# Kernel optimization log

Measured on AMD Instinct MI355X. Metric: run time of the kernel, lower is better.

The kernel has to match this reference:

```python
import jax, jax.numpy as jnp
import numpy as np

H = 300  # hidden size hardcoded in the module
VX = 32000
VY = 32000
NX, NY, B = 128, 128, 256


def setup_inputs() -> dict:
    key = jax.random.key(0)
    ks = jax.random.split(key, 10)
    s = 1.0 / np.sqrt(H)
    x = jax.random.randint(ks[0], (NX, B), 0, VX)
    y = jax.random.randint(ks[1], (NY, B), 0, VY)
    # padding_idx=0: zero the pad row of each embedding table
    enc_emb = jax.random.normal(ks[2], (VX, H), jnp.float32).at[0].set(0.0)
    encW = jax.random.uniform(ks[3], (H, H), jnp.float32, -s, s)
    encb = jax.random.uniform(ks[4], (H,), jnp.float32, -s, s)
    dec_emb = jax.random.normal(ks[5], (VY, H), jnp.float32).at[0].set(0.0)
    decW = jax.random.uniform(ks[6], (H, H), jnp.float32, -s, s)
    decb = jax.random.uniform(ks[7], (H,), jnp.float32, -s, s)
    outW = jax.random.uniform(ks[8], (VY, H), jnp.float32, -s, s)
    outb = jax.random.uniform(ks[9], (VY,), jnp.float32, -s, s)
    return {"x": x, "y": y, "enc_emb": enc_emb, "encW": encW, "encb": encb,
            "dec_emb": dec_emb, "decW": decW, "decb": decb,
            "outW": outW, "outb": outb}


def reference(x, y, enc_emb, encW, encb, dec_emb, decW, decb, outW, outb):
    # Encoder: Elman recurrence h = relu(e_x[i] + W h + b)
    e_x = enc_emb[x]                                  # [NX, B, H]
    h0 = jnp.zeros((x.shape[1], H), e_x.dtype)        # h=0 broadcast over batch

    def enc_step(h, ex):
        return jax.nn.relu(ex + h @ encW.T + encb), None

    h, _ = jax.lax.scan(enc_step, h0, e_x)

    # Decoder: teacher-forced recurrence with per-step mean cross-entropy
    e_y = dec_emb[y]                                  # [NY, B, H]

    def dec_step(h, inp):
        ey, tgt = inp
        h = jax.nn.relu(ey + h @ decW.T + decb)
        logits = h @ outW.T + outb                    # [B, VY]
        logp = jax.nn.log_softmax(logits, axis=-1)
        ce = -jnp.mean(jnp.take_along_axis(logp, tgt[:, None], axis=-1))
        return h, ce

    _, ces = jax.lax.scan(dec_step, h, (e_y[:-1], y[1:]))
    return jnp.sum(ces)
```

## Files before the change

kernel.cpp:

```cpp
#include <hip/hip_runtime.h>
#include <hip/hip_bf16.h>
#include <stdint.h>

typedef unsigned short u16;
typedef unsigned char u8;
typedef float f32x4 __attribute__((ext_vector_type(4)));
typedef float f32x2 __attribute__((ext_vector_type(2)));
typedef _Float16 f16x2 __attribute__((ext_vector_type(2)));
typedef _Float16 f16x8 __attribute__((ext_vector_type(8)));

#define H      300
#define KP     320
#define BATCH  256
#define NX     128
#define NY     128
#define VY     32000
#define NPAD   32768
#define MROWS  32512


#define OWS_OFF   0UL
#define OWS_BYTES ((unsigned long)NPAD * KP)
#define OWS_PAD   131072UL
#define A8_OFF    (OWS_OFF + OWS_BYTES + OWS_PAD)
#define A8_BYTES  ((unsigned long)MROWS * KP)
#define WTE_OFF   (A8_OFF + A8_BYTES)
#define WT_BYTES  (320UL * KP * 4)
#define WTD_OFF   (WTE_OFF + WT_BYTES)
#define OBP_OFF   (WTD_OFF + WT_BYTES)
#define OBP_BYTES ((unsigned long)NPAD * 4)
#define SE_OFF    (OBP_OFF + OBP_BYTES)
#define SE_BYTES  ((unsigned long)MROWS * 4)
#define EE_OFF    (SE_OFF + SE_BYTES)
#define E1_BYTES  ((unsigned long)NX * BATCH * 320 * 2)
#define ED_OFF    (EE_OFF + E1_BYTES)
#define WS_NEED   (ED_OFF + E1_BYTES)

#define ASYNC_COPY16(dst_lds, src_glb)                                          \
    __builtin_amdgcn_global_load_lds(                                           \
        (const __attribute__((address_space(1))) unsigned int*)(src_glb),       \
        (__attribute__((address_space(3))) unsigned int*)(dst_lds), 16, 0, 0)

__global__ __launch_bounds__(256) void k0_prep(const float* __restrict__ outW,
                                               const float* __restrict__ encW,
                                               const float* __restrict__ decW,
                                               const float* __restrict__ outb,
                                               u8* __restrict__ ows,
                                               float* __restrict__ eob,
                                               float* __restrict__ wte,
                                               float* __restrict__ wtd) {
    long id = (long)blockIdx.x * 256 + threadIdx.x;
    const long n1 = (long)NPAD * KP / 4;
    if (id < n1) {
        int v = (int)(id / 80), k4 = (int)(id % 80) * 4;
        float4 f = {0.f, 0.f, 0.f, 0.f};
        if (v < VY && k4 < H) f = *(const float4*)&outW[(long)v * H + k4];
        int w = __builtin_amdgcn_cvt_pk_fp8_f32(f.x, f.y, 0, false);
        w = __builtin_amdgcn_cvt_pk_fp8_f32(f.z, f.w, w, true);
        long dst = (long)(v >> 6) * 20480 + (k4 >> 5) * 2048 + ((v >> 4) & 3) * 512
                 + (v & 15) * 8 + ((k4 >> 3) & 3) * 128 + (k4 & 7);
        *(unsigned int*)(ows + dst) = (unsigned int)w;
        return;
    }
    long id2 = id - n1;
    if (id2 < NPAD) {
        eob[id2] = (id2 < VY) ? __expf(outb[id2]) : 0.f;
        return;
    }
    id2 -= NPAD;
    if (id2 < 320L * KP) {
        int k = (int)(id2 / KP), j = (int)(id2 % KP);
        wte[id2] = (k < H && j < H) ? encW[j * H + k] : 0.f;
        return;
    }
    id2 -= 320L * KP;
    if (id2 < 320L * KP) {
        int k = (int)(id2 / KP), j = (int)(id2 % KP);
        wtd[id2] = (k < H && j < H) ? decW[j * H + k] : 0.f;
    }
}

__global__ __launch_bounds__(256) void k0b_emb(const int* __restrict__ x,
                                               const int* __restrict__ y,
                                               const float* __restrict__ enc_emb,
                                               const float* __restrict__ dec_emb,
                                               const float* __restrict__ encb,
                                               const float* __restrict__ decb,
                                               _Float16* __restrict__ Ee,
                                               _Float16* __restrict__ Ed) {
    long id = (long)blockIdx.x * 256 + threadIdx.x;
    const long NE = (long)NX * BATCH * 320;
    bool isenc = id < NE;
    long id2 = isenc ? id : id - NE;
    if (id2 >= NE) return;
    int t = (int)(id2 / (BATCH * 320));
    int r = (int)(id2 % (BATCH * 320));
    int b = r / 320, j = r % 320;
    if (isenc) {
        int ix = x[t * BATCH + b];
        float v = (j < H) ? enc_emb[(long)ix * H + j] + encb[j] : 0.f;
        Ee[id2] = (_Float16)v;
    } else {
        int iy = y[t * BATCH + b];
        float v = (j < H) ? dec_emb[(long)iy * H + j] + decb[j] : 0.f;
        Ed[id2] = (_Float16)v;
    }
}

template <int PRE>
__global__ __launch_bounds__(640) void k1_rnn(const int* __restrict__ x,
                                              const int* __restrict__ y,
                                              const float* __restrict__ enc_emb,
                                              const float* __restrict__ dec_emb,
                                              const float* __restrict__ encb,
                                              const float* __restrict__ decb,
                                              const float* __restrict__ wte,
                                              const float* __restrict__ wtd,
                                              const _Float16* __restrict__ Ee,
                                              const _Float16* __restrict__ Ed,
                                              u8* __restrict__ A8) {
    const int tid = threadIdx.x;
    const int s = tid / 160;
    const int j = tid - s * 160;
    const int b = blockIdx.x;

    __shared__ __align__(16) _Float16 hh[320];
    __shared__ float part[1280];
    __shared__ __align__(4) u8 a8row[320];

    for (int i = tid; i < 320; i += 640) hh[i] = (_Float16)0.f;

    const bool comb = (tid < 320);
    const int jc = tid;
    const float be = (!PRE && comb && jc < H) ? encb[jc] : 0.f;
    const float bd = (!PRE && comb && jc < H) ? decb[jc] : 0.f;

    f16x2 wa[40], wc[40];
#pragma unroll
    for (int kk = 0; kk < 40; ++kk) {
        int k0 = s * 80 + 2 * kk;
        wa[kk] = (f16x2){(_Float16)wte[k0 * KP + j],       (_Float16)wte[(k0 + 1) * KP + j]};
        wc[kk] = (f16x2){(_Float16)wte[k0 * KP + j + 160], (_Float16)wte[(k0 + 1) * KP + j + 160]};
    }

    int idx_n = PRE ? 0 : x[BATCH + b];
    float e_cur = 0.f;
    if (comb) {
        if (PRE) e_cur = (float)Ee[(long)b * 320 + jc];
        else if (jc < H) e_cur = enc_emb[(long)x[b] * H + jc];
    }
    __syncthreads();

    const f16x8* hb8 = (const f16x8*)&hh[s * 80];

    for (int t = 0; t < NX; ++t) {
        float e_nx = 0.f;
        int idx_n2 = 0;
        if (PRE) {
            if (comb && t + 1 < NX)
                e_nx = (float)Ee[((long)(t + 1) * BATCH + b) * 320 + jc];
        } else {
            idx_n2 = x[min(t + 2, NX - 1) * BATCH + b];
            if (comb && jc < H && t + 1 < NX) e_nx = enc_emb[(long)idx_n * H + jc];
        }

        float p0 = 0.f, p1 = 0.f;
#pragma unroll
        for (int i = 0; i < 10; ++i) {
            f16x8 hv = hb8[i];
            f16x2 q0 = {hv[0], hv[1]}, q1 = {hv[2], hv[3]};
            f16x2 q2 = {hv[4], hv[5]}, q3 = {hv[6], hv[7]};
            p0 = __builtin_amdgcn_fdot2(wa[4 * i + 0], q0, p0, false);
            p1 = __builtin_amdgcn_fdot2(wc[4 * i + 0], q0, p1, false);
            p0 = __builtin_amdgcn_fdot2(wa[4 * i + 1], q1, p0, false);
            p1 = __builtin_amdgcn_fdot2(wc[4 * i + 1], q1, p1, false);
            p0 = __builtin_amdgcn_fdot2(wa[4 * i + 2], q2, p0, false);
            p1 = __builtin_amdgcn_fdot2(wc[4 * i + 2], q2, p1, false);
            p0 = __builtin_amdgcn_fdot2(wa[4 * i + 3], q3, p0, false);
            p1 = __builtin_amdgcn_fdot2(wc[4 * i + 3], q3, p1, false);
        }
        part[s * 320 + j] = p0;
        part[s * 320 + 160 + j] = p1;
        __syncthreads();
        if (comb) {
            float v = part[jc] + part[320 + jc] + part[640 + jc] + part[960 + jc] + be + e_cur;
            hh[jc] = (_Float16)fmaxf(v, 0.f);
        }
        __syncthreads();
        e_cur = e_nx; idx_n = idx_n2;
    }

#pragma unroll
    for (int kk = 0; kk < 40; ++kk) {
        int k0 = s * 80 + 2 * kk;
        wa[kk] = (f16x2){(_Float16)wtd[k0 * KP + j],       (_Float16)wtd[(k0 + 1) * KP + j]};
        wc[kk] = (f16x2){(_Float16)wtd[k0 * KP + j + 160], (_Float16)wtd[(k0 + 1) * KP + j + 160]};
    }

    idx_n = PRE ? 0 : y[BATCH + b];
    e_cur = 0.f;
    if (comb) {
        if (PRE) e_cur = (float)Ed[(long)b * 320 + jc];
        else if (jc < H) e_cur = dec_emb[(long)y[b] * H + jc];
    }

    for (int t = 0; t < NY - 1; ++t) {
        float e_nx = 0.f;
        int idx_n2 = 0;
        if (PRE) {
            if (comb && t + 1 < NY - 1)
                e_nx = (float)Ed[((long)(t + 1) * BATCH + b) * 320 + jc];
        } else {
            idx_n2 = y[min(t + 2, NY - 1) * BATCH + b];
            if (comb && jc < H && t + 1 < NY - 1) e_nx = dec_emb[(long)idx_n * H + jc];
        }

        float p0 = 0.f, p1 = 0.f;
#pragma unroll
        for (int i = 0; i < 10; ++i) {
            f16x8 hv = hb8[i];
            f16x2 q0 = {hv[0], hv[1]}, q1 = {hv[2], hv[3]};
            f16x2 q2 = {hv[4], hv[5]}, q3 = {hv[6], hv[7]};
            p0 = __builtin_amdgcn_fdot2(wa[4 * i + 0], q0, p0, false);
            p1 = __builtin_amdgcn_fdot2(wc[4 * i + 0], q0, p1, false);
            p0 = __builtin_amdgcn_fdot2(wa[4 * i + 1], q1, p0, false);
            p1 = __builtin_amdgcn_fdot2(wc[4 * i + 1], q1, p1, false);
            p0 = __builtin_amdgcn_fdot2(wa[4 * i + 2], q2, p0, false);
            p1 = __builtin_amdgcn_fdot2(wc[4 * i + 2], q2, p1, false);
            p0 = __builtin_amdgcn_fdot2(wa[4 * i + 3], q3, p0, false);
            p1 = __builtin_amdgcn_fdot2(wc[4 * i + 3], q3, p1, false);
        }
        part[s * 320 + j] = p0;
        part[s * 320 + 160 + j] = p1;
        __syncthreads();
        if (comb) {
            float v = part[jc] + part[320 + jc] + part[640 + jc] + part[960 + jc] + bd + e_cur;
            v = fmaxf(v, 0.f);
            hh[jc] = (_Float16)v;
            int pk = __builtin_amdgcn_cvt_pk_fp8_f32(v, v, 0, false);
            a8row[jc] = (u8)(pk & 0xff);
        }
        __syncthreads();
        if (tid < 80)
            ((unsigned int*)(A8 + (long)(t * BATCH + b) * KP))[tid] =
                ((const unsigned int*)a8row)[tid];
        e_cur = e_nx; idx_n = idx_n2;
    }
}

__global__ __launch_bounds__(256, 2) void k2_gemm(const u8* __restrict__ A8,
                                                  const u8* __restrict__ OWS,
                                                  const float* __restrict__ eob,
                                                  float* __restrict__ sumexp) {
    const int tid = threadIdx.x;
    const int lane = tid & 63, wave = tid >> 6;
    const int lane16 = lane & 15, quad = lane >> 4;
    const int bid = blockIdx.x;
    const int cg8 = bid & 7;
    const int cs  = (bid >> 3) & 3;
    const int rb  = bid >> 5;
    const int colbase = cg8 * 4096 + cs * 1024;
    const long tile0 = (long)(colbase >> 6);

    __shared__ __align__(16) u8 bt[2][20480];

    long a[4][10];
    {
        const u8* abase = A8 + ((long)rb * 256 + wave * 64 + lane16) * KP + quad * 8;
#pragma unroll
        for (int rt = 0; rt < 4; ++rt)
#pragma unroll
            for (int ks = 0; ks < 10; ++ks)
                a[rt][ks] = *(const long*)(abase + rt * 16 * KP + ks * 32);
    }

    {
        const u8* src = OWS + tile0 * 20480 + (wave << 10) + (lane << 4);
        u8* dst = &bt[0][wave << 10];
#pragma unroll
        for (int r = 0; r < 5; ++r)
            ASYNC_COPY16(dst + r * 4096, src + r * 4096);
    }

    float rsum[16];
#pragma unroll
    for (int i = 0; i < 16; ++i) rsum[i] = 0.f;

    f32x4 accLo[4][2], accHi[4][2];

#pragma unroll 1
    for (int ct = 0; ct < 16; ++ct) {
        __syncthreads();
        if (ct < 15) {
            const u8* src = OWS + (tile0 + ct + 1) * 20480 + (wave << 10) + (lane << 4);
            u8* dst = &bt[(ct + 1) & 1][wave << 10];
#pragma unroll
            for (int r = 0; r < 5; ++r)
                ASYNC_COPY16(dst + r * 4096, src + r * 4096);
        }
        const u8* bb = &bt[ct & 1][0];

#pragma unroll
        for (int p = 0; p < 4; ++p)
#pragma unroll
            for (int q = 0; q < 2; ++q) accLo[p][q] = (f32x4){0.f, 0.f, 0.f, 0.f};
#pragma unroll
        for (int ks = 0; ks < 10; ++ks) {
            long b0 = *(const long*)(bb + ks * 2048 + 0 * 512 + lane * 8);
            long b1 = *(const long*)(bb + ks * 2048 + 1 * 512 + lane * 8);
#pragma unroll
            for (int rt = 0; rt < 4; ++rt) {
                accLo[rt][0] = __builtin_amdgcn_mfma_f32_16x16x32_fp8_fp8(
                    a[rt][ks], b0, accLo[rt][0], 0, 0, 0);
                accLo[rt][1] = __builtin_amdgcn_mfma_f32_16x16x32_fp8_fp8(
                    a[rt][ks], b1, accLo[rt][1], 0, 0, 0);
            }
        }
        if (ct > 0) {
            int cbp = colbase + (ct - 1) * 64;
#pragma unroll
            for (int tc = 0; tc < 2; ++tc) {
                float eb = eob[cbp + (tc + 2) * 16 + lane16];
#pragma unroll
                for (int rt = 0; rt < 4; ++rt)
#pragma unroll
                    for (int i = 0; i < 4; ++i)
                        rsum[rt * 4 + i] += __expf(accHi[rt][tc][i]) * eb;
            }
        }

#pragma unroll
        for (int p = 0; p < 4; ++p)
#pragma unroll
            for (int q = 0; q < 2; ++q) accHi[p][q] = (f32x4){0.f, 0.f, 0.f, 0.f};
#pragma unroll
        for (int ks = 0; ks < 10; ++ks) {
            long b2 = *(const long*)(bb + ks * 2048 + 2 * 512 + lane * 8);
            long b3 = *(const long*)(bb + ks * 2048 + 3 * 512 + lane * 8);
#pragma unroll
            for (int rt = 0; rt < 4; ++rt) {
                accHi[rt][0] = __builtin_amdgcn_mfma_f32_16x16x32_fp8_fp8(
                    a[rt][ks], b2, accHi[rt][0], 0, 0, 0);
                accHi[rt][1] = __builtin_amdgcn_mfma_f32_16x16x32_fp8_fp8(
                    a[rt][ks], b3, accHi[rt][1], 0, 0, 0);
            }
        }
        {
            int cb = colbase + ct * 64;
#pragma unroll
            for (int tc = 0; tc < 2; ++tc) {
                float eb = eob[cb + tc * 16 + lane16];
#pragma unroll
                for (int rt = 0; rt < 4; ++rt)
#pragma unroll
                    for (int i = 0; i < 4; ++i)
                        rsum[rt * 4 + i] += __expf(accLo[rt][tc][i]) * eb;
            }
        }
    }

    {
        int cb = colbase + 15 * 64;
#pragma unroll
        for (int tc = 0; tc < 2; ++tc) {
            float eb = eob[cb + (tc + 2) * 16 + lane16];
#pragma unroll
            for (int rt = 0; rt < 4; ++rt)
#pragma unroll
                for (int i = 0; i < 4; ++i)
                    rsum[rt * 4 + i] += __expf(accHi[rt][tc][i]) * eb;
        }
    }

#pragma unroll
    for (int m = 1; m < 16; m <<= 1)
#pragma unroll
        for (int i = 0; i < 16; ++i) rsum[i] += __shfl_xor(rsum[i], m, 64);
    if (lane16 == 0) {
        float* sp = &sumexp[(long)rb * 256 + wave * 64];
#pragma unroll
        for (int rt = 0; rt < 4; ++rt)
#pragma unroll
            for (int i = 0; i < 4; ++i)
                atomicAdd(&sp[rt * 16 + quad * 4 + i], rsum[rt * 4 + i]);
    }
}

__global__ __launch_bounds__(256) void k3_ce(const u8* __restrict__ A8,
                                             const u8* __restrict__ OWS,
                                             const float* __restrict__ outb,
                                             const float* __restrict__ sumexp,
                                             const int* __restrict__ y,
                                             float* __restrict__ out) {
    const int wave = threadIdx.x >> 6, lane = threadIdx.x & 63;
    const int r = blockIdx.x * 4 + wave;
    const int t = r >> 8, b = r & 255;
    const int tgt = y[(t + 1) * BATCH + b];
    float s = 0.f;
    if (lane < 40) {
        unsigned long long av = *(const unsigned long long*)(A8 + (long)r * KP + lane * 8);
        long wdst = (long)(tgt >> 6) * 20480 + (lane >> 2) * 2048
                  + ((tgt >> 4) & 3) * 512 + (tgt & 15) * 8 + (lane & 3) * 128;
        unsigned long long wv = *(const unsigned long long*)(OWS + wdst);
        unsigned int a4 = (unsigned int)av, a4h = (unsigned int)(av >> 32);
        unsigned int w4 = (unsigned int)wv, w4h = (unsigned int)(wv >> 32);
        f32x2 al = __builtin_amdgcn_cvt_pk_f32_fp8(a4, false);
        f32x2 ah = __builtin_amdgcn_cvt_pk_f32_fp8(a4, true);
        f32x2 wl = __builtin_amdgcn_cvt_pk_f32_fp8(w4, false);
        f32x2 wh = __builtin_amdgcn_cvt_pk_f32_fp8(w4, true);
        s += al[0] * wl[0] + al[1] * wl[1] + ah[0] * wh[0] + ah[1] * wh[1];
        al = __builtin_amdgcn_cvt_pk_f32_fp8(a4h, false);
        ah = __builtin_amdgcn_cvt_pk_f32_fp8(a4h, true);
        wl = __builtin_amdgcn_cvt_pk_f32_fp8(w4h, false);
        wh = __builtin_amdgcn_cvt_pk_f32_fp8(w4h, true);
        s += al[0] * wl[0] + al[1] * wl[1] + ah[0] * wh[0] + ah[1] * wh[1];
    }
#pragma unroll
    for (int m = 1; m < 64; m <<= 1) s += __shfl_xor(s, m, 64);
    __shared__ float part[4];
    if (lane == 0) part[wave] = logf(sumexp[r]) - (s + outb[tgt]);
    __syncthreads();
    if (threadIdx.x == 0) {
        float tot = part[0] + part[1] + part[2] + part[3];
        atomicAdd(out, tot * (1.0f / 256.0f));
    }
}

extern "C" void kernel_launch(void* const* d_in, const int* in_sizes, int n_in,
                              void* d_out, int out_size, void* d_ws, size_t ws_size,
                              hipStream_t stream) {
    (void)in_sizes; (void)n_in; (void)out_size;
    const int*   x       = (const int*)d_in[0];
    const int*   y       = (const int*)d_in[1];
    const float* enc_emb = (const float*)d_in[2];
    const float* encW    = (const float*)d_in[3];
    const float* encb    = (const float*)d_in[4];
    const float* dec_emb = (const float*)d_in[5];
    const float* decW    = (const float*)d_in[6];
    const float* decb    = (const float*)d_in[7];
    const float* outW    = (const float*)d_in[8];
    const float* outb    = (const float*)d_in[9];

    char* ws = (char*)d_ws;
    u8* ows  = (u8*)(ws + OWS_OFF);
    u8* A8   = (u8*)(ws + A8_OFF);
    float* wte    = (float*)(ws + WTE_OFF);
    float* wtd    = (float*)(ws + WTD_OFF);
    float* eob    = (float*)(ws + OBP_OFF);
    float* sumexp = (float*)(ws + SE_OFF);
    _Float16* Ee  = (_Float16*)(ws + EE_OFF);
    _Float16* Ed  = (_Float16*)(ws + ED_OFF);

    hipMemsetAsync(sumexp, 0, SE_BYTES, stream);
    hipMemsetAsync(d_out, 0, sizeof(float), stream);

    long n0 = (long)NPAD * KP / 4 + NPAD + 2L * 320 * KP;
    k0_prep<<<(int)((n0 + 255) / 256), 256, 0, stream>>>(outW, encW, decW, outb,
                                                         ows, eob, wte, wtd);
    const bool pre = (ws_size >= WS_NEED);
    if (pre) {
        long ne = 2L * NX * BATCH * 320;
        k0b_emb<<<(int)((ne + 255) / 256), 256, 0, stream>>>(x, y, enc_emb, dec_emb,
                                                             encb, decb, Ee, Ed);
        k1_rnn<1><<<256, 640, 0, stream>>>(x, y, enc_emb, dec_emb, encb, decb,
                                           wte, wtd, Ee, Ed, A8);
    } else {
        k1_rnn<0><<<256, 640, 0, stream>>>(x, y, enc_emb, dec_emb, encb, decb,
                                           wte, wtd, Ee, Ed, A8);
    }
    k2_gemm<<<127 * 32, 256, 0, stream>>>(A8, ows, eob, sumexp);
    k3_ce<<<8128, 256, 0, stream>>>(A8, ows, outb, sumexp, y, (float*)d_out);
}
```

Baseline: 970.4 us.

## Restructure RNN recurrence to wave-shuffle reductions with double-buffered state

The recurrent kernel now splits the K dimension across lane groups within a wave and reduces partial dot products with cross-lane shuffles instead of a shared-memory partial buffer. The hidden state and fp8 row are double-buffered, so each step needs one barrier instead of two, and the write of the activation row to global memory is deferred to the next step. Separately, the fp8 output-weight layout is interleaved so the GEMM loads both B fragments with one 16-byte load instead of two 8-byte loads, and the CE kernel's indexing is updated to match. The main target is the serialized per-step latency of the recurrence, at the cost of more complex indexing.

```diff
diff --git a/kernel.cpp b/kernel.cpp
--- a/kernel.cpp
+++ b/kernel.cpp
@@ -8,6 +8,7 @@
 typedef float f32x2 __attribute__((ext_vector_type(2)));
 typedef _Float16 f16x2 __attribute__((ext_vector_type(2)));
 typedef _Float16 f16x8 __attribute__((ext_vector_type(8)));
+typedef long lx2 __attribute__((ext_vector_type(2)));
 
 #define H      300
 #define KP     320
@@ -57,8 +58,9 @@
         if (v < VY && k4 < H) f = *(const float4*)&outW[(long)v * H + k4];
         int w = __builtin_amdgcn_cvt_pk_fp8_f32(f.x, f.y, 0, false);
         w = __builtin_amdgcn_cvt_pk_fp8_f32(f.z, f.w, w, true);
-        long dst = (long)(v >> 6) * 20480 + (k4 >> 5) * 2048 + ((v >> 4) & 3) * 512
-                 + (v & 15) * 8 + ((k4 >> 3) & 3) * 128 + (k4 & 7);
+        int laneb = (v & 15) + ((k4 >> 3) & 3) * 16;
+        long dst = (long)(v >> 6) * 20480 + (k4 >> 5) * 2048 + ((v >> 5) & 1) * 1024
+                 + (long)laneb * 16 + ((v >> 4) & 1) * 8 + (k4 & 7);
         *(unsigned int*)(ows + dst) = (unsigned int)w;
         return;
     }
@@ -120,50 +122,60 @@
                                               const _Float16* __restrict__ Ed,
                                               u8* __restrict__ A8) {
     const int tid = threadIdx.x;
-    const int s = tid / 160;
-    const int j = tid - s * 160;
+    const int wave = tid >> 6, lane = tid & 63;
+    const int lane16 = lane & 15;
+    const int kb = (lane >> 4) * 80;
     const int b = blockIdx.x;
-
-    __shared__ __align__(16) _Float16 hh[320];
-    __shared__ float part[1280];
-    __shared__ __align__(4) u8 a8row[320];
-
-    for (int i = tid; i < 320; i += 640) hh[i] = (_Float16)0.f;
-
-    const bool comb = (tid < 320);
-    const int jc = tid;
-    const float be = (!PRE && comb && jc < H) ? encb[jc] : 0.f;
-    const float bd = (!PRE && comb && jc < H) ? decb[jc] : 0.f;
+    const int c0 = wave * 32 + lane16 * 2, c1 = c0 + 1;
+    const bool red = (lane < 16);
+
+    __shared__ __align__(16) _Float16 hh2[2][320];
+    __shared__ __align__(4)  u8 a8row[2][320];
+
+    ((_Float16*)hh2)[tid] = (_Float16)0.f;
 
     f16x2 wa[40], wc[40];
 #pragma unroll
     for (int kk = 0; kk < 40; ++kk) {
-        int k0 = s * 80 + 2 * kk;
-        wa[kk] = (f16x2){(_Float16)wte[k0 * KP + j],       (_Float16)wte[(k0 + 1) * KP + j]};
-        wc[kk] = (f16x2){(_Float16)wte[k0 * KP + j + 160], (_Float16)wte[(k0 + 1) * KP + j + 160]};
-    }
-
-    int idx_n = PRE ? 0 : x[BATCH + b];
-    float e_cur = 0.f;
-    if (comb) {
-        if (PRE) e_cur = (float)Ee[(long)b * 320 + jc];
-        else if (jc < H) e_cur = enc_emb[(long)x[b] * H + jc];
-    }
+        int k0 = kb + 2 * kk;
+        wa[kk] = (f16x2){(_Float16)wte[k0 * KP + c0], (_Float16)wte[(k0 + 1) * KP + c0]};
+        wc[kk] = (f16x2){(_Float16)wte[k0 * KP + c1], (_Float16)wte[(k0 + 1) * KP + c1]};
+    }
+
+    const float be0 = (!PRE && red && c0 < H) ? encb[c0] : 0.f;
+    const float be1 = (!PRE && red && c1 < H) ? encb[c1] : 0.f;
+
+    int idx_n = 0;
+    float e0 = 0.f, e1 = 0.f;
+    if (red) {
+        if (PRE) {
+            f16x2 ev = *(const f16x2*)&Ee[(long)b * 320 + c0];
+            e0 = (float)ev[0]; e1 = (float)ev[1];
+        } else {
+            int i0 = x[b];
+            if (c0 < H) e0 = enc_emb[(long)i0 * H + c0];
+            if (c1 < H) e1 = enc_emb[(long)i0 * H + c1];
+        }
+    }
+    if (!PRE) idx_n = x[BATCH + b];
     __syncthreads();
 
-    const f16x8* hb8 = (const f16x8*)&hh[s * 80];
-
+#pragma unroll 1
     for (int t = 0; t < NX; ++t) {
-        float e_nx = 0.f;
+        float en0 = 0.f, en1 = 0.f;
         int idx_n2 = 0;
-        if (PRE) {
-            if (comb && t + 1 < NX)
-                e_nx = (float)Ee[((long)(t + 1) * BATCH + b) * 320 + jc];
-        } else {
-            idx_n2 = x[min(t + 2, NX - 1) * BATCH + b];
-            if (comb && jc < H && t + 1 < NX) e_nx = enc_emb[(long)idx_n * H + jc];
-        }
-
+        if (red && t + 1 < NX) {
+            if (PRE) {
+                f16x2 ev = *(const f16x2*)&Ee[((long)(t + 1) * BATCH + b) * 320 + c0];
+                en0 = (float)ev[0]; en1 = (float)ev[1];
+            } else {
+                if (c0 < H) en0 = enc_emb[(long)idx_n * H + c0];
+                if (c1 < H) en1 = enc_emb[(long)idx_n * H + c1];
+            }
+        }
+        if (!PRE) idx_n2 = x[min(t + 2, NX - 1) * BATCH + b];
+
+        const f16x8* hb8 = (const f16x8*)&hh2[t & 1][kb];
         float p0 = 0.f, p1 = 0.f;
 #pragma unroll
         for (int i = 0; i < 10; ++i) {
@@ -179,42 +191,58 @@
             p0 = __builtin_amdgcn_fdot2(wa[4 * i + 3], q3, p0, false);
             p1 = __builtin_amdgcn_fdot2(wc[4 * i + 3], q3, p1, false);
         }
-        part[s * 320 + j] = p0;
-        part[s * 320 + 160 + j] = p1;
+        p0 += __shfl_xor(p0, 16, 64); p0 += __shfl_xor(p0, 32, 64);
+        p1 += __shfl_xor(p1, 16, 64); p1 += __shfl_xor(p1, 32, 64);
+        if (red) {
+            float v0 = fmaxf(p0 + be0 + e0, 0.f);
+            float v1 = fmaxf(p1 + be1 + e1, 0.f);
+            *(f16x2*)&hh2[(t + 1) & 1][c0] = (f16x2){(_Float16)v0, (_Float16)v1};
+        }
         __syncthreads();
-        if (comb) {
-            float v = part[jc] + part[320 + jc] + part[640 + jc] + part[960 + jc] + be + e_cur;
-            hh[jc] = (_Float16)fmaxf(v, 0.f);
-        }
-        __syncthreads();
-        e_cur = e_nx; idx_n = idx_n2;
+        e0 = en0; e1 = en1; idx_n = idx_n2;
     }
 
 #pragma unroll
     for (int kk = 0; kk < 40; ++kk) {
-        int k0 = s * 80 + 2 * kk;
-        wa[kk] = (f16x2){(_Float16)wtd[k0 * KP + j],       (_Float16)wtd[(k0 + 1) * KP + j]};
-        wc[kk] = (f16x2){(_Float16)wtd[k0 * KP + j + 160], (_Float16)wtd[(k0 + 1) * KP + j + 160]};
-    }
-
-    idx_n = PRE ? 0 : y[BATCH + b];
-    e_cur = 0.f;
-    if (comb) {
-        if (PRE) e_cur = (float)Ed[(long)b * 320 + jc];
-        else if (jc < H) e_cur = dec_emb[(long)y[b] * H + jc];
-    }
-
+        int k0 = kb + 2 * kk;
+        wa[kk] = (f16x2){(_Float16)wtd[k0 * KP + c0], (_Float16)wtd[(k0 + 1) * KP + c0]};
+        wc[kk] = (f16x2){(_Float16)wtd[k0 * KP + c1], (_Float16)wtd[(k0 + 1) * KP + c1]};
+    }
+    const float bd0 = (!PRE && red && c0 < H) ? decb[c0] : 0.f;
+    const float bd1 = (!PRE && red && c1 < H) ? decb[c1] : 0.f;
+    e0 = 0.f; e1 = 0.f;
+    if (red) {
+        if (PRE) {
+            f16x2 ev = *(const f16x2*)&Ed[(long)b * 320 + c0];
+            e0 = (float)ev[0]; e1 = (float)ev[1];
+        } else {
+            int i0 = y[b];
+            if (c0 < H) e0 = dec_emb[(long)i0 * H + c0];
+            if (c1 < H) e1 = dec_emb[(long)i0 * H + c1];
+        }
+    }
+    if (!PRE) idx_n = y[BATCH + b];
+
+#pragma unroll 1
     for (int t = 0; t < NY - 1; ++t) {
-        float e_nx = 0.f;
+        if (t > 0 && tid < 80)
+            ((unsigned int*)(A8 + (long)((t - 1) * BATCH + b) * KP))[tid] =
+                ((const unsigned int*)a8row[(t - 1) & 1])[tid];
+
+        float en0 = 0.f, en1 = 0.f;
         int idx_n2 = 0;
-        if (PRE) {
-            if (comb && t + 1 < NY - 1)
-                e_nx = (float)Ed[((long)(t + 1) * BATCH + b) * 320 + jc];
-        } else {
-            idx_n2 = y[min(t + 2, NY - 1) * BATCH + b];
-            if (comb && jc < H && t + 1 < NY - 1) e_nx = dec_emb[(long)idx_n * H + jc];
-        }
-
+        if (red && t + 1 < NY - 1) {
+            if (PRE) {
+                f16x2 ev = *(const f16x2*)&Ed[((long)(t + 1) * BATCH + b) * 320 + c0];
+                en0 = (float)ev[0]; en1 = (float)ev[1];
+            } else {
+                if (c0 < H) en0 = dec_emb[(long)idx_n * H + c0];
+                if (c1 < H) en1 = dec_emb[(long)idx_n * H + c1];
+            }
+        }
+        if (!PRE) idx_n2 = y[min(t + 2, NY - 1) * BATCH + b];
+
+        const f16x8* hb8 = (const f16x8*)&hh2[t & 1][kb];
         float p0 = 0.f, p1 = 0.f;
 #pragma unroll
         for (int i = 0; i < 10; ++i) {
@@ -230,22 +258,22 @@
             p0 = __builtin_amdgcn_fdot2(wa[4 * i + 3], q3, p0, false);
             p1 = __builtin_amdgcn_fdot2(wc[4 * i + 3], q3, p1, false);
         }
-        part[s * 320 + j] = p0;
-        part[s * 320 + 160 + j] = p1;
+        p0 += __shfl_xor(p0, 16, 64); p0 += __shfl_xor(p0, 32, 64);
+        p1 += __shfl_xor(p1, 16, 64); p1 += __shfl_xor(p1, 32, 64);
+        if (red) {
+            float v0 = fmaxf(p0 + bd0 + e0, 0.f);
+            float v1 = fmaxf(p1 + bd1 + e1, 0.f);
+            *(f16x2*)&hh2[(t + 1) & 1][c0] = (f16x2){(_Float16)v0, (_Float16)v1};
+            int pk = __builtin_amdgcn_cvt_pk_fp8_f32(v0, v1, 0, false);
+            *(u16*)&a8row[t & 1][c0] = (u16)(pk & 0xffff);
+        }
         __syncthreads();
-        if (comb) {
-            float v = part[jc] + part[320 + jc] + part[640 + jc] + part[960 + jc] + bd + e_cur;
-            v = fmaxf(v, 0.f);
-            hh[jc] = (_Float16)v;
-            int pk = __builtin_amdgcn_cvt_pk_fp8_f32(v, v, 0, false);
-            a8row[jc] = (u8)(pk & 0xff);
-        }
-        __syncthreads();
-        if (tid < 80)
-            ((unsigned int*)(A8 + (long)(t * BATCH + b) * KP))[tid] =
-                ((const unsigned int*)a8row)[tid];
-        e_cur = e_nx; idx_n = idx_n2;
-    }
+        e0 = en0; e1 = en1; idx_n = idx_n2;
+    }
+
+    if (tid < 80)
+        ((unsigned int*)(A8 + (long)((NY - 2) * BATCH + b) * KP))[tid] =
+            ((const unsigned int*)a8row[(NY - 2) & 1])[tid];
 }
 
 __global__ __launch_bounds__(256, 2) void k2_gemm(const u8* __restrict__ A8,
@@ -306,14 +334,13 @@
             for (int q = 0; q < 2; ++q) accLo[p][q] = (f32x4){0.f, 0.f, 0.f, 0.f};
 #pragma unroll
         for (int ks = 0; ks < 10; ++ks) {
-            long b0 = *(const long*)(bb + ks * 2048 + 0 * 512 + lane * 8);
-            long b1 = *(const long*)(bb + ks * 2048 + 1 * 512 + lane * 8);
+            lx2 bp = *(const lx2*)(bb + ks * 2048 + lane * 16);
 #pragma unroll
             for (int rt = 0; rt < 4; ++rt) {
                 accLo[rt][0] = __builtin_amdgcn_mfma_f32_16x16x32_fp8_fp8(
-                    a[rt][ks], b0, accLo[rt][0], 0, 0, 0);
+                    a[rt][ks], bp[0], accLo[rt][0], 0, 0, 0);
                 accLo[rt][1] = __builtin_amdgcn_mfma_f32_16x16x32_fp8_fp8(
-                    a[rt][ks], b1, accLo[rt][1], 0, 0, 0);
+                    a[rt][ks], bp[1], accLo[rt][1], 0, 0, 0);
             }
         }
         if (ct > 0) {
@@ -335,14 +362,13 @@
             for (int q = 0; q < 2; ++q) accHi[p][q] = (f32x4){0.f, 0.f, 0.f, 0.f};
 #pragma unroll
         for (int ks = 0; ks < 10; ++ks) {
-            long b2 = *(const long*)(bb + ks * 2048 + 2 * 512 + lane * 8);
-            long b3 = *(const long*)(bb + ks * 2048 + 3 * 512 + lane * 8);
+            lx2 bp = *(const lx2*)(bb + ks * 2048 + 1024 + lane * 16);
 #pragma unroll
             for (int rt = 0; rt < 4; ++rt) {
                 accHi[rt][0] = __builtin_amdgcn_mfma_f32_16x16x32_fp8_fp8(
-                    a[rt][ks], b2, accHi[rt][0], 0, 0, 0);
+                    a[rt][ks], bp[0], accHi[rt][0], 0, 0, 0);
                 accHi[rt][1] = __builtin_amdgcn_mfma_f32_16x16x32_fp8_fp8(
-                    a[rt][ks], b3, accHi[rt][1], 0, 0, 0);
+                    a[rt][ks], bp[1], accHi[rt][1], 0, 0, 0);
             }
         }
         {
@@ -399,8 +425,9 @@
     float s = 0.f;
     if (lane < 40) {
         unsigned long long av = *(const unsigned long long*)(A8 + (long)r * KP + lane * 8);
+        int laneb = (tgt & 15) + (lane & 3) * 16;
         long wdst = (long)(tgt >> 6) * 20480 + (lane >> 2) * 2048
-                  + ((tgt >> 4) & 3) * 512 + (tgt & 15) * 8 + (lane & 3) * 128;
+                  + ((tgt >> 5) & 1) * 1024 + (long)laneb * 16 + ((tgt >> 4) & 1) * 8;
         unsigned long long wv = *(const unsigned long long*)(OWS + wdst);
         unsigned int a4 = (unsigned int)av, a4h = (unsigned int)(av >> 32);
         unsigned int w4 = (unsigned int)wv, w4h = (unsigned int)(wv >> 32);
```

Measured after the change: 1.038 ms. 6.9% more time.
